# Optimization experiments

Hardware: AMD Instinct MI355X
Metric: run time of the kernel (lower is better)

The kernel has to match this reference:

```python
import jax, jax.numpy as jnp
import numpy as np

B, S, F, H = 4, 1024, 512, 16
D = F // H  # head_dim = 32

def setup_inputs() -> dict:
    key = jax.random.key(0)
    ks = jax.random.split(key, 9)
    init = lambda k, shp: 0.1 * jax.random.normal(k, shp, dtype=jnp.float32)
    return {
        "kv": jax.random.normal(ks[0], (B, S, F), dtype=jnp.float32),
        "q": jax.random.normal(ks[1], (B, S, F), dtype=jnp.float32),
        "mask": jnp.ones((B, 1, S, S), dtype=jnp.int32),
        "Wq": init(ks[2], (F, F)),
        "Wk": init(ks[3], (F, F)),
        "Wv": init(ks[4], (F, F)),
        "Wo": init(ks[5], (F, F)),
        "rel_table": init(ks[6], (2 * S + 1, D)),  # nn.Embed(2*length_q+1, head_dim)
        "Wrel": init(ks[7], (D, D)),  # rel_pos_dense, no bias
    }

def reference(kv, q, mask, Wq, Wk, Wv, Wo, rel_table, Wrel):
    b, s, f = q.shape
    h, d = H, f // H
    qh = (q @ Wq).reshape(b, s, h, d)
    kh = (kv @ Wk).reshape(b, s, h, d)
    vh = (kv @ Wv).reshape(b, s, h, d)
    # raw content scores [b,h,q,k]
    scores = jnp.einsum('bqhd,bkhd->bhqk', qh, kh)
    # relative-position embedding: dist in [0, 2s], table lookup + dense
    dist = jnp.arange(s)[None, :] - jnp.arange(s)[:, None] + s  # [q,k]
    emb = rel_table[dist] @ Wrel  # [q,k,d]
    scores = scores + jnp.einsum('bqhd,qkd->bhqk', qh, emb)
    scores = scores / jnp.sqrt(jnp.asarray(d, scores.dtype))
    # mask-select before softmax (mask [b,1,q,k] broadcast over heads)
    scores = jnp.where(mask > 0, scores, -jnp.inf)
    attn = jax.nn.softmax(scores, axis=-1)
    out = jnp.einsum('bhqk,bkhd->bqhd', attn, vh).reshape(b, s, f)
    return out @ Wo  # dropout is identity (training=False)
```

## Files before the change

kernel.cpp:

```cpp
#include <hip/hip_runtime.h>

#define S_ 1024
#define H_ 16
#define D_ 32

typedef float f32x4 __attribute__((ext_vector_type(4)));
typedef short bf16x8 __attribute__((ext_vector_type(8)));
typedef unsigned long long u64;

static __device__ __forceinline__ short f2b(float f) {
    union { float f; unsigned u; } x; x.f = f;
    unsigned u = x.u;
    unsigned r = u + 0x7fffu + ((u >> 16) & 1u);
    return (short)(r >> 16);
}
static __device__ __forceinline__ unsigned pk_rne(float lo, float hi) {
    union { float f; unsigned u; } a, b; a.f = lo; b.f = hi;
    unsigned ul = a.u + 0x7fffu + ((a.u >> 16) & 1u);
    unsigned uh = b.u + 0x7fffu + ((b.u >> 16) & 1u);
    return __builtin_amdgcn_perm(uh, ul, 0x07060302u);
}
static __device__ __forceinline__ unsigned pk_trunc(float lo, float hi) {
    union { float f; unsigned u; } a, b; a.f = lo; b.f = hi;
    return __builtin_amdgcn_perm(b.u, a.u, 0x07060302u);
}
static __device__ __forceinline__ float bperm(int bidx, float v) {
    union { float f; int i; } x; x.f = v;
    x.i = __builtin_amdgcn_ds_bpermute(bidx, x.i);
    return x.f;
}
static __device__ __forceinline__ int stg64(int row, int c8) {
    return row * 72 + (c8 ^ ((row & 3) << 3));
}

__global__ __launch_bounds__(256)
void prep_kernel(const float* __restrict__ rt, short* __restrict__ relb,
                 const int* __restrict__ mask, u64* __restrict__ mbits,
                 const float* __restrict__ Wq, const float* __restrict__ Wk,
                 const float* __restrict__ Wv, const float* __restrict__ Wo,
                 short* __restrict__ Wt)
{
    __shared__ float ls[32][33];
    int bid = blockIdx.x, t = threadIdx.x;
    if (bid < 257) {
        int i = bid * 256 + t;
        if (i < 2049 * 32) relb[i] = f2b(rt[i]);
        return;
    }
    bid -= 257;
    if (bid < 4096) {
        #pragma unroll
        for (int j = 0; j < 4; ++j) {
            int i = bid * 1024 + j * 256 + t;
            u64 bal = __ballot(mask[i] > 0);
            if ((t & 63) == 0) mbits[i >> 6] = bal;
        }
        return;
    }
    bid -= 4096;
    int mat = bid >> 8, tl = bid & 255, ti = tl >> 4, tj = tl & 15;
    const float* W = (mat == 0) ? Wq : (mat == 1) ? Wk : (mat == 2) ? Wv : Wo;
    int r = t >> 3, c = (t & 7) * 4;
    float4 v = *(const float4*)(W + (long)(ti * 32 + r) * 512 + tj * 32 + c);
    ls[r][c] = v.x; ls[r][c + 1] = v.y; ls[r][c + 2] = v.z; ls[r][c + 3] = v.w;
    __syncthreads();
    int nl = t >> 3, kk = (t & 7) * 4;
    uint2 o = { pk_rne(ls[kk][nl], ls[kk + 1][nl]),
                pk_rne(ls[kk + 2][nl], ls[kk + 3][nl]) };
    *(uint2*)(Wt + ((long)mat * 512 + tj * 32 + nl) * 512 + ti * 32 + kk) = o;
}

__global__ __launch_bounds__(256)
void gemm3_kernel(const float* __restrict__ q, const float* __restrict__ kv,
                  const short* __restrict__ Wt,
                  short* __restrict__ qh, short* __restrict__ kh, short* __restrict__ vt,
                  float scale)
{
    __shared__ __align__(16) short a_s[128 * 72];
    __shared__ __align__(16) short b_s[64 * 72];
    const int t = threadIdx.x;
    const int w = t >> 6, lane = t & 63, l15 = lane & 15, quad = lane >> 4;
    const int wm = w & 1, wn = w >> 1;

    int bid = blockIdx.x;
    const int mat = bid >> 8;
    const int rr_ = bid & 255;
    const int bmr = (rr_ & 31) * 128, bnr = (rr_ >> 5) * 64;
    const float* A = (mat == 0) ? q : kv;
    const short* Wm = Wt + (long)mat * 262144;

    const int srow = t >> 2, scg = (t & 3) << 4;
    f32x4 acc[8] = {};

    for (int k0 = 0; k0 < 512; k0 += 64) {
        #pragma unroll
        for (int hp = 0; hp < 2; ++hp) {
            int row = hp * 64 + srow;
            const float* ap = A + (long)(bmr + row) * 512 + k0 + scg;
            float4 v0 = *(const float4*)(ap);
            float4 v1 = *(const float4*)(ap + 4);
            float4 v2 = *(const float4*)(ap + 8);
            float4 v3 = *(const float4*)(ap + 12);
            uint4 o0 = { pk_rne(v0.x, v0.y), pk_rne(v0.z, v0.w),
                         pk_rne(v1.x, v1.y), pk_rne(v1.z, v1.w) };
            uint4 o1 = { pk_rne(v2.x, v2.y), pk_rne(v2.z, v2.w),
                         pk_rne(v3.x, v3.y), pk_rne(v3.z, v3.w) };
            *(uint4*)(a_s + stg64(row, scg)) = o0;
            *(uint4*)(a_s + stg64(row, scg + 8)) = o1;
        }
        {
            const short* bp = Wm + (long)(bnr + srow) * 512 + k0 + scg;
            *(bf16x8*)(b_s + stg64(srow, scg))     = *(const bf16x8*)(bp);
            *(bf16x8*)(b_s + stg64(srow, scg + 8)) = *(const bf16x8*)(bp + 8);
        }
        __syncthreads();
        bf16x8 af[4][2], bfr[2][2];
        #pragma unroll
        for (int ks = 0; ks < 2; ++ks) {
            #pragma unroll
            for (int i = 0; i < 4; ++i)
                af[i][ks] = *(const bf16x8*)(a_s + stg64(wm * 64 + i * 16 + l15, ks * 32 + quad * 8));
            #pragma unroll
            for (int j = 0; j < 2; ++j)
                bfr[j][ks] = *(const bf16x8*)(b_s + stg64(wn * 32 + j * 16 + l15, ks * 32 + quad * 8));
        }
        if (mat == 2) {
            #pragma unroll
            for (int i = 0; i < 2; ++i)
                #pragma unroll
                for (int j = 0; j < 4; ++j)
                    #pragma unroll
                    for (int ks = 0; ks < 2; ++ks)
                        acc[i * 4 + j] = __builtin_amdgcn_mfma_f32_16x16x32_bf16(bfr[i][ks], af[j][ks], acc[i * 4 + j], 0, 0, 0);
        } else {
            #pragma unroll
            for (int i = 0; i < 4; ++i)
                #pragma unroll
                for (int j = 0; j < 2; ++j)
                    #pragma unroll
                    for (int ks = 0; ks < 2; ++ks)
                        acc[i * 2 + j] = __builtin_amdgcn_mfma_f32_16x16x32_bf16(af[i][ks], bfr[j][ks], acc[i * 2 + j], 0, 0, 0);
        }
        __syncthreads();
    }

    if (mat < 2) {
        short* out = (mat == 0) ? qh : kh;
        float alpha = (mat == 0) ? scale : 1.0f;
        #pragma unroll
        for (int i = 0; i < 4; ++i)
            #pragma unroll
            for (int j = 0; j < 2; ++j)
                #pragma unroll
                for (int r = 0; r < 4; ++r) {
                    int m = bmr + wm * 64 + i * 16 + quad * 4 + r;
                    int n = bnr + wn * 32 + j * 16 + l15;
                    int bb = m >> 10, s = m & 1023, hh = n >> 5, dd = n & 31;
                    out[((long)((bb * 16 + hh) * 1024 + s)) * 32 + dd] = f2b(acc[i * 2 + j][r] * alpha);
                }
    } else {
        #pragma unroll
        for (int i = 0; i < 2; ++i)
            #pragma unroll
            for (int j = 0; j < 4; ++j)
                #pragma unroll
                for (int r = 0; r < 4; ++r) {
                    int n = bnr + wn * 32 + i * 16 + quad * 4 + r;
                    int m = bmr + wm * 64 + j * 16 + l15;
                    int bb = m >> 10, s = m & 1023, hh = n >> 5, dd = n & 31;
                    int sp = (s & ~63) | ((s & 15) << 2) | ((s >> 4) & 3);
                    vt[((long)((bb * 16 + hh) * 32 + dd)) * 1024 + sp] = f2b(acc[i * 4 + j][r]);
                }
    }
}

__global__ __launch_bounds__(256)
void gemm_out_kernel(const short* __restrict__ ao, const short* __restrict__ Wt,
                     float* __restrict__ out)
{
    __shared__ __align__(16) short a_s[64 * 72];
    __shared__ __align__(16) short b_s[64 * 72];
    const int t = threadIdx.x;
    const int w = t >> 6, lane = t & 63, l15 = lane & 15, quad = lane >> 4;
    const int wm = w & 1, wn = w >> 1;
    const int bm = (blockIdx.x & 63) * 64, bn = (blockIdx.x >> 6) * 64;
    const short* Wm = Wt + (long)3 * 262144;
    const int srow = t >> 2, scg = (t & 3) << 4;
    f32x4 acc[2][2] = {};

    for (int k0 = 0; k0 < 512; k0 += 64) {
        {
            const short* apb = ao + (long)(bm + srow) * 512 + k0 + scg;
            *(bf16x8*)(a_s + stg64(srow, scg))     = *(const bf16x8*)(apb);
            *(bf16x8*)(a_s + stg64(srow, scg + 8)) = *(const bf16x8*)(apb + 8);
            const short* bpb = Wm + (long)(bn + srow) * 512 + k0 + scg;
            *(bf16x8*)(b_s + stg64(srow, scg))     = *(const bf16x8*)(bpb);
            *(bf16x8*)(b_s + stg64(srow, scg + 8)) = *(const bf16x8*)(bpb + 8);
        }
        __syncthreads();
        bf16x8 af[2][2], bfr[2][2];
        #pragma unroll
        for (int i = 0; i < 2; ++i)
            #pragma unroll
            for (int ks = 0; ks < 2; ++ks) {
                af[i][ks]  = *(const bf16x8*)(a_s + stg64(wm * 32 + i * 16 + l15, ks * 32 + quad * 8));
                bfr[i][ks] = *(const bf16x8*)(b_s + stg64(wn * 32 + i * 16 + l15, ks * 32 + quad * 8));
            }
        #pragma unroll
        for (int i = 0; i < 2; ++i)
            #pragma unroll
            for (int j = 0; j < 2; ++j)
                #pragma unroll
                for (int ks = 0; ks < 2; ++ks)
                    acc[i][j] = __builtin_amdgcn_mfma_f32_16x16x32_bf16(af[i][ks], bfr[j][ks], acc[i][j], 0, 0, 0);
        __syncthreads();
    }
    #pragma unroll
    for (int i = 0; i < 2; ++i)
        #pragma unroll
        for (int j = 0; j < 2; ++j)
            #pragma unroll
            for (int r = 0; r < 4; ++r) {
                int m = bm + wm * 32 + i * 16 + quad * 4 + r;
                int n = bn + wn * 32 + j * 16 + l15;
                out[(long)m * 512 + n] = acc[i][j][r];
            }
}

__global__ __launch_bounds__(256)
void attn_kernel(const short* __restrict__ qh, const float* __restrict__ wrel,
                 const short* __restrict__ kh, const short* __restrict__ vt,
                 const short* __restrict__ relb, const u64* __restrict__ mbits,
                 short* __restrict__ ao)
{
    __shared__ __align__(16) short smem[4 * 2 * 16 * 72];
    const int t = threadIdx.x;
    const int w = t >> 6, lane = t & 63, l15 = lane & 15, quad = lane >> 4;
    short* pw0 = smem + w * (2 * 16 * 72);
    short* pw1 = pw0 + 16 * 72;

    const int half = w & 1, qsel = w >> 1;
    const int bid = blockIdx.x;
    const int xcd = bid & 7, loc = bid >> 3;
    const int bh = xcd + 8 * (loc >> 5);
    const int qt = (loc & 31) * 2 + qsel;
    const int b = bh >> 4, h = bh & 15;
    const int q0 = qt * 16;
    const int c0 = half * 8;

    const long qbase = ((long)bh * S_ + q0 + l15) * D_ + quad * 8;
    const bf16x8 a_qh = *(const bf16x8*)(qh + qbase);
    const long kv_bh = (long)bh * S_ * D_;
    const u64* mrow = mbits + ((long)b * S_ + q0 + quad * 4) * 16;

    bf16x8 a_qr;
    {
        #pragma unroll
        for (int nt = 0; nt < 2; ++nt) {
            const float* wp = wrel + (long)(nt * 16 + l15) * 32 + quad * 8;
            float4 w0 = *(const float4*)(wp);
            float4 w1 = *(const float4*)(wp + 4);
            bf16x8 bw;
            *(uint4*)&bw = (uint4){ pk_rne(w0.x, w0.y), pk_rne(w0.z, w0.w),
                                    pk_rne(w1.x, w1.y), pk_rne(w1.z, w1.w) };
            f32x4 z = {0.f, 0.f, 0.f, 0.f};
            f32x4 cq = __builtin_amdgcn_mfma_f32_16x16x32_bf16(a_qh, bw, z, 0, 0, 0);
            #pragma unroll
            for (int r = 0; r < 4; ++r)
                pw0[(quad * 4 + r) * 36 + nt * 16 + l15] = f2b(cq[r]);
        }
        asm volatile("" ::: "memory");
        a_qr = *(const bf16x8*)(pw0 + l15 * 36 + quad * 8);
        asm volatile("" ::: "memory");
    }

    int bidx[4];
    #pragma unroll
    for (int r = 0; r < 4; ++r)
        bidx[r] = (quad * 16 + ((l15 + 15 - (quad * 4 + r)) & 15)) * 4;

    f32x4 oacc[2] = {};
    float l4[4] = {0.f, 0.f, 0.f, 0.f};

    bf16x8 preg0 = {}, preg1 = {};
    bf16x8 bv00 = {}, bv01 = {}, bv10 = {}, bv11 = {};

    bf16x8 kf[4], rf[5];
    {
        const int ub0 = c0 * 64 - q0 + (S_ - 15);
        #pragma unroll
        for (int ut = 0; ut < 5; ++ut)
            rf[ut] = *(const bf16x8*)(relb + (long)(ub0 + ut * 16 + l15) * D_ + quad * 8);
        #pragma unroll
        for (int kt = 0; kt < 4; ++kt)
            kf[kt] = *(const bf16x8*)(kh + kv_bh + (long)(c0 * 64 + kt * 16 + l15) * D_ + quad * 8);
    }

    for (int i = 0; i < 8; ++i) {
        const int c = c0 + i;
        const int kbase = c * 64;
        short* pwbuf = (i & 1) ? pw1 : pw0;

        u64 mcur[4];
        #pragma unroll
        for (int r = 0; r < 4; ++r) mcur[r] = mrow[r * 16 + c];

        f32x4 ctf[5], sc[4];
        #pragma unroll
        for (int ut = 0; ut < 5; ++ut) {
            f32x4 z = {0.f, 0.f, 0.f, 0.f};
            ctf[ut] = __builtin_amdgcn_mfma_f32_16x16x32_bf16(a_qr, rf[ut], z, 0, 0, 0);
        }
        #pragma unroll
        for (int kt = 0; kt < 4; ++kt) {
            f32x4 z = {0.f, 0.f, 0.f, 0.f};
            sc[kt] = __builtin_amdgcn_mfma_f32_16x16x32_bf16(a_qh, kf[kt], z, 0, 0, 0);
        }
        if (i) {
            oacc[0] = __builtin_amdgcn_mfma_f32_16x16x32_bf16(preg0, bv00, oacc[0], 0, 0, 0);
            oacc[1] = __builtin_amdgcn_mfma_f32_16x16x32_bf16(preg0, bv01, oacc[1], 0, 0, 0);
            oacc[0] = __builtin_amdgcn_mfma_f32_16x16x32_bf16(preg1, bv10, oacc[0], 0, 0, 0);
            oacc[1] = __builtin_amdgcn_mfma_f32_16x16x32_bf16(preg1, bv11, oacc[1], 0, 0, 0);
        }
        {
            const int cn = c + ((i < 7) ? 1 : 0);
            const int kbn = cn * 64, ubn = kbn - q0 + (S_ - 15);
            #pragma unroll
            for (int ut = 0; ut < 5; ++ut)
                rf[ut] = *(const bf16x8*)(relb + (long)(ubn + ut * 16 + l15) * D_ + quad * 8);
            #pragma unroll
            for (int kt = 0; kt < 4; ++kt)
                kf[kt] = *(const bf16x8*)(kh + kv_bh + (long)(kbn + kt * 16 + l15) * D_ + quad * 8);
        }
        bv00 = *(const bf16x8*)(vt + kv_bh + (long)(l15) * S_ + kbase + quad * 8);
        bv01 = *(const bf16x8*)(vt + kv_bh + (long)(16 + l15) * S_ + kbase + quad * 8);
        bv10 = *(const bf16x8*)(vt + kv_bh + (long)(l15) * S_ + kbase + 32 + quad * 8);
        bv11 = *(const bf16x8*)(vt + kv_bh + (long)(16 + l15) * S_ + kbase + 32 + quad * 8);

        #pragma unroll
        for (int r = 0; r < 4; ++r) {
            int cnd = l15 > quad * 4 + r;
            float tt[5];
            #pragma unroll
            for (int ut = 0; ut < 5; ++ut) tt[ut] = bperm(bidx[r], ctf[ut][r]);
            float s0 = sc[0][r] + (cnd ? tt[1] : tt[0]);
            float s1 = sc[1][r] + (cnd ? tt[2] : tt[1]);
            float s2 = sc[2][r] + (cnd ? tt[3] : tt[2]);
            float s3 = sc[3][r] + (cnd ? tt[4] : tt[3]);
            u64 mw = mcur[r] >> l15;
            unsigned lo = (unsigned)mw, hi = (unsigned)(mw >> 32);
            float p0 = exp2f(s0); p0 = (lo & 1u)         ? p0 : 0.f;
            float p1 = exp2f(s1); p1 = ((lo >> 16) & 1u) ? p1 : 0.f;
            float p2 = exp2f(s2); p2 = (hi & 1u)         ? p2 : 0.f;
            float p3 = exp2f(s3); p3 = ((hi >> 16) & 1u) ? p3 : 0.f;
            l4[r] += (p0 + p1) + (p2 + p3);
            u64 pv = ((u64)pk_trunc(p2, p3) << 32) | (u64)pk_trunc(p0, p1);
            *(u64*)(pwbuf + (quad * 4 + r) * 72 + l15 * 4) = pv;
        }
        asm volatile("" ::: "memory");
        preg0 = *(const bf16x8*)(pwbuf + l15 * 72 + quad * 8);
        preg1 = *(const bf16x8*)(pwbuf + l15 * 72 + 32 + quad * 8);
    }
    oacc[0] = __builtin_amdgcn_mfma_f32_16x16x32_bf16(preg0, bv00, oacc[0], 0, 0, 0);
    oacc[1] = __builtin_amdgcn_mfma_f32_16x16x32_bf16(preg0, bv01, oacc[1], 0, 0, 0);
    oacc[0] = __builtin_amdgcn_mfma_f32_16x16x32_bf16(preg1, bv10, oacc[0], 0, 0, 0);
    oacc[1] = __builtin_amdgcn_mfma_f32_16x16x32_bf16(preg1, bv11, oacc[1], 0, 0, 0);

    #pragma unroll
    for (int r = 0; r < 4; ++r) {
        float l = l4[r];
        l += __shfl_xor(l, 1, 64);
        l += __shfl_xor(l, 2, 64);
        l += __shfl_xor(l, 4, 64);
        l += __shfl_xor(l, 8, 64);
        l4[r] = l;
    }

    asm volatile("" ::: "memory");
    float* fo = (float*)pw0;
    float* fl = (float*)pw1;
    #pragma unroll
    for (int r = 0; r < 4; ++r) {
        #pragma unroll
        for (int dt = 0; dt < 2; ++dt)
            fo[(quad * 4 + r) * 32 + dt * 16 + l15] = oacc[dt][r];
        if (l15 == 0) fl[quad * 4 + r] = l4[r];
    }
    __syncthreads();
    if (half == 0) {
        const float* po = (const float*)(smem + (w ^ 1) * (2 * 16 * 72));
        const float* pl = po + 576;
        #pragma unroll
        for (int r = 0; r < 4; ++r) {
            int row = quad * 4 + r;
            float inv = 1.0f / (l4[r] + pl[row]);
            #pragma unroll
            for (int dt = 0; dt < 2; ++dt) {
                float o = oacc[dt][r] + po[row * 32 + dt * 16 + l15];
                ao[((long)(b * S_ + q0 + row) * H_ + h) * D_ + dt * 16 + l15] = f2b(o * inv);
            }
        }
    }
}

extern "C" void kernel_launch(void* const* d_in, const int* in_sizes, int n_in,
                              void* d_out, int out_size, void* d_ws, size_t ws_size,
                              hipStream_t stream) {
    (void)in_sizes; (void)n_in; (void)out_size; (void)ws_size;
    const float* kv   = (const float*)d_in[0];
    const float* q    = (const float*)d_in[1];
    const int*   mask = (const int*)d_in[2];
    const float* Wq   = (const float*)d_in[3];
    const float* Wk   = (const float*)d_in[4];
    const float* Wv   = (const float*)d_in[5];
    const float* Wo   = (const float*)d_in[6];
    const float* rt   = (const float*)d_in[7];
    const float* Wrel = (const float*)d_in[8];

    char* ws = (char*)d_ws;
    short* qh   = (short*)(ws);
    short* kh   = (short*)(ws + (4u  << 20));
    short* vt   = (short*)(ws + (8u  << 20));
    short* ao   = (short*)(ws + (12u << 20));
    short* Wt   = (short*)(ws + (16u << 20));
    short* relb = (short*)(ws + (18u << 20));
    u64*  mbits = (u64*) (ws + (18u << 20) + (256u << 10));

    const float scale = 0.25503486f;

    prep_kernel<<<257 + 4096 + 1024, 256, 0, stream>>>(
        rt, relb, mask, mbits, Wq, Wk, Wv, Wo, Wt);

    gemm3_kernel<<<768, 256, 0, stream>>>(q, kv, Wt, qh, kh, vt, scale);

    attn_kernel<<<2048, 256, 0, stream>>>(qh, Wrel, kh, vt, relb, mbits, ao);

    gemm_out_kernel<<<512, 256, 0, stream>>>(ao, Wt, (float*)d_out);
}
```

Baseline: 193.3 us.

## Fuse K and V projections per block, enlarge output GEMM tile, simplify attention mapping

The QKV projection kernel now computes K and V together in one block, so the kv activation tile is loaded and converted to bf16 once instead of twice. This cuts the grid from 768 to 512 blocks, with 256 q-blocks and 256 heavier kv-blocks, which leaves the load unbalanced. The output GEMM switches to 128x64 tiles, halving its blocks to raise reuse of the shared-memory tile at the cost of fewer blocks in flight. The attention kernel drops the XCD-aware block remapping for a linear one and reads mask words inline rather than preloading them into registers.

```diff
diff --git a/kernel.cpp b/kernel.cpp
--- a/kernel.cpp
+++ b/kernel.cpp
@@ -77,20 +77,21 @@
                   float scale)
 {
     __shared__ __align__(16) short a_s[128 * 72];
-    __shared__ __align__(16) short b_s[64 * 72];
+    __shared__ __align__(16) short bk_s[64 * 72];
+    __shared__ __align__(16) short bv_s[64 * 72];
     const int t = threadIdx.x;
     const int w = t >> 6, lane = t & 63, l15 = lane & 15, quad = lane >> 4;
     const int wm = w & 1, wn = w >> 1;
 
-    int bid = blockIdx.x;
-    const int mat = bid >> 8;
-    const int rr_ = bid & 255;
-    const int bmr = (rr_ & 31) * 128, bnr = (rr_ >> 5) * 64;
-    const float* A = (mat == 0) ? q : kv;
-    const short* Wm = Wt + (long)mat * 262144;
+    const int bid = blockIdx.x;
+    const int isq = (bid < 256);
+    const int x = isq ? bid : bid - 256;
+    const int bmr = (x & 31) * 128, bnr = (x >> 5) * 64;
+    const float* A = isq ? q : kv;
 
     const int srow = t >> 2, scg = (t & 3) << 4;
     f32x4 acc[8] = {};
+    f32x4 acv[8] = {};
 
     for (int k0 = 0; k0 < 512; k0 += 64) {
         #pragma unroll
@@ -108,13 +109,20 @@
             *(uint4*)(a_s + stg64(row, scg)) = o0;
             *(uint4*)(a_s + stg64(row, scg + 8)) = o1;
         }
-        {
-            const short* bp = Wm + (long)(bnr + srow) * 512 + k0 + scg;
-            *(bf16x8*)(b_s + stg64(srow, scg))     = *(const bf16x8*)(bp);
-            *(bf16x8*)(b_s + stg64(srow, scg + 8)) = *(const bf16x8*)(bp + 8);
+        if (isq) {
+            const short* bp = Wt + (long)(bnr + srow) * 512 + k0 + scg;
+            *(bf16x8*)(bk_s + stg64(srow, scg))     = *(const bf16x8*)(bp);
+            *(bf16x8*)(bk_s + stg64(srow, scg + 8)) = *(const bf16x8*)(bp + 8);
+        } else {
+            const short* bpk = Wt + 262144 + (long)(bnr + srow) * 512 + k0 + scg;
+            const short* bpv = Wt + 2 * 262144 + (long)(bnr + srow) * 512 + k0 + scg;
+            *(bf16x8*)(bk_s + stg64(srow, scg))     = *(const bf16x8*)(bpk);
+            *(bf16x8*)(bk_s + stg64(srow, scg + 8)) = *(const bf16x8*)(bpk + 8);
+            *(bf16x8*)(bv_s + stg64(srow, scg))     = *(const bf16x8*)(bpv);
+            *(bf16x8*)(bv_s + stg64(srow, scg + 8)) = *(const bf16x8*)(bpv + 8);
         }
         __syncthreads();
-        bf16x8 af[4][2], bfr[2][2];
+        bf16x8 af[4][2], bk[2][2];
         #pragma unroll
         for (int ks = 0; ks < 2; ++ks) {
             #pragma unroll
@@ -122,31 +130,36 @@
                 af[i][ks] = *(const bf16x8*)(a_s + stg64(wm * 64 + i * 16 + l15, ks * 32 + quad * 8));
             #pragma unroll
             for (int j = 0; j < 2; ++j)
-                bfr[j][ks] = *(const bf16x8*)(b_s + stg64(wn * 32 + j * 16 + l15, ks * 32 + quad * 8));
-        }
-        if (mat == 2) {
+                bk[j][ks] = *(const bf16x8*)(bk_s + stg64(wn * 32 + j * 16 + l15, ks * 32 + quad * 8));
+        }
+        #pragma unroll
+        for (int i = 0; i < 4; ++i)
+            #pragma unroll
+            for (int j = 0; j < 2; ++j)
+                #pragma unroll
+                for (int ks = 0; ks < 2; ++ks)
+                    acc[i * 2 + j] = __builtin_amdgcn_mfma_f32_16x16x32_bf16(af[i][ks], bk[j][ks], acc[i * 2 + j], 0, 0, 0);
+        if (!isq) {
+            bf16x8 bv_[2][2];
+            #pragma unroll
+            for (int ks = 0; ks < 2; ++ks)
+                #pragma unroll
+                for (int j = 0; j < 2; ++j)
+                    bv_[j][ks] = *(const bf16x8*)(bv_s + stg64(wn * 32 + j * 16 + l15, ks * 32 + quad * 8));
             #pragma unroll
             for (int i = 0; i < 2; ++i)
                 #pragma unroll
                 for (int j = 0; j < 4; ++j)
                     #pragma unroll
                     for (int ks = 0; ks < 2; ++ks)
-                        acc[i * 4 + j] = __builtin_amdgcn_mfma_f32_16x16x32_bf16(bfr[i][ks], af[j][ks], acc[i * 4 + j], 0, 0, 0);
-        } else {
-            #pragma unroll
-            for (int i = 0; i < 4; ++i)
-                #pragma unroll
-                for (int j = 0; j < 2; ++j)
-                    #pragma unroll
-                    for (int ks = 0; ks < 2; ++ks)
-                        acc[i * 2 + j] = __builtin_amdgcn_mfma_f32_16x16x32_bf16(af[i][ks], bfr[j][ks], acc[i * 2 + j], 0, 0, 0);
+                        acv[i * 4 + j] = __builtin_amdgcn_mfma_f32_16x16x32_bf16(bv_[i][ks], af[j][ks], acv[i * 4 + j], 0, 0, 0);
         }
         __syncthreads();
     }
 
-    if (mat < 2) {
-        short* out = (mat == 0) ? qh : kh;
-        float alpha = (mat == 0) ? scale : 1.0f;
+    {
+        short* out = isq ? qh : kh;
+        float alpha = isq ? scale : 1.0f;
         #pragma unroll
         for (int i = 0; i < 4; ++i)
             #pragma unroll
@@ -158,7 +171,8 @@
                     int bb = m >> 10, s = m & 1023, hh = n >> 5, dd = n & 31;
                     out[((long)((bb * 16 + hh) * 1024 + s)) * 32 + dd] = f2b(acc[i * 2 + j][r] * alpha);
                 }
-    } else {
+    }
+    if (!isq) {
         #pragma unroll
         for (int i = 0; i < 2; ++i)
             #pragma unroll
@@ -169,7 +183,7 @@
                     int m = bmr + wm * 64 + j * 16 + l15;
                     int bb = m >> 10, s = m & 1023, hh = n >> 5, dd = n & 31;
                     int sp = (s & ~63) | ((s & 15) << 2) | ((s >> 4) & 3);
-                    vt[((long)((bb * 16 + hh) * 32 + dd)) * 1024 + sp] = f2b(acc[i * 4 + j][r]);
+                    vt[((long)((bb * 16 + hh) * 32 + dd)) * 1024 + sp] = f2b(acv[i * 4 + j][r]);
                 }
     }
 }
@@ -178,52 +192,58 @@
 void gemm_out_kernel(const short* __restrict__ ao, const short* __restrict__ Wt,
                      float* __restrict__ out)
 {
-    __shared__ __align__(16) short a_s[64 * 72];
+    __shared__ __align__(16) short a_s[128 * 72];
     __shared__ __align__(16) short b_s[64 * 72];
     const int t = threadIdx.x;
     const int w = t >> 6, lane = t & 63, l15 = lane & 15, quad = lane >> 4;
     const int wm = w & 1, wn = w >> 1;
-    const int bm = (blockIdx.x & 63) * 64, bn = (blockIdx.x >> 6) * 64;
+    const int bm = (blockIdx.x & 31) * 128, bn = (blockIdx.x >> 5) * 64;
     const short* Wm = Wt + (long)3 * 262144;
     const int srow = t >> 2, scg = (t & 3) << 4;
-    f32x4 acc[2][2] = {};
+    f32x4 acc[8] = {};
 
     for (int k0 = 0; k0 < 512; k0 += 64) {
+        #pragma unroll
+        for (int hp = 0; hp < 2; ++hp) {
+            int row = hp * 64 + srow;
+            const short* apb = ao + (long)(bm + row) * 512 + k0 + scg;
+            *(bf16x8*)(a_s + stg64(row, scg))     = *(const bf16x8*)(apb);
+            *(bf16x8*)(a_s + stg64(row, scg + 8)) = *(const bf16x8*)(apb + 8);
+        }
         {
-            const short* apb = ao + (long)(bm + srow) * 512 + k0 + scg;
-            *(bf16x8*)(a_s + stg64(srow, scg))     = *(const bf16x8*)(apb);
-            *(bf16x8*)(a_s + stg64(srow, scg + 8)) = *(const bf16x8*)(apb + 8);
             const short* bpb = Wm + (long)(bn + srow) * 512 + k0 + scg;
             *(bf16x8*)(b_s + stg64(srow, scg))     = *(const bf16x8*)(bpb);
             *(bf16x8*)(b_s + stg64(srow, scg + 8)) = *(const bf16x8*)(bpb + 8);
         }
         __syncthreads();
-        bf16x8 af[2][2], bfr[2][2];
-        #pragma unroll
-        for (int i = 0; i < 2; ++i)
-            #pragma unroll
-            for (int ks = 0; ks < 2; ++ks) {
-                af[i][ks]  = *(const bf16x8*)(a_s + stg64(wm * 32 + i * 16 + l15, ks * 32 + quad * 8));
-                bfr[i][ks] = *(const bf16x8*)(b_s + stg64(wn * 32 + i * 16 + l15, ks * 32 + quad * 8));
-            }
-        #pragma unroll
-        for (int i = 0; i < 2; ++i)
+        bf16x8 af[4][2], bfr[2][2];
+        #pragma unroll
+        for (int ks = 0; ks < 2; ++ks) {
+            #pragma unroll
+            for (int i = 0; i < 4; ++i)
+                af[i][ks] = *(const bf16x8*)(a_s + stg64(wm * 64 + i * 16 + l15, ks * 32 + quad * 8));
             #pragma unroll
             for (int j = 0; j < 2; ++j)
+                bfr[j][ks] = *(const bf16x8*)(b_s + stg64(wn * 32 + j * 16 + l15, ks * 32 + quad * 8));
+        }
+        #pragma unroll
+        for (int i = 0; i < 4; ++i)
+            #pragma unroll
+            for (int j = 0; j < 2; ++j)
                 #pragma unroll
                 for (int ks = 0; ks < 2; ++ks)
-                    acc[i][j] = __builtin_amdgcn_mfma_f32_16x16x32_bf16(af[i][ks], bfr[j][ks], acc[i][j], 0, 0, 0);
+                    acc[i * 2 + j] = __builtin_amdgcn_mfma_f32_16x16x32_bf16(af[i][ks], bfr[j][ks], acc[i * 2 + j], 0, 0, 0);
         __syncthreads();
     }
     #pragma unroll
-    for (int i = 0; i < 2; ++i)
+    for (int i = 0; i < 4; ++i)
         #pragma unroll
         for (int j = 0; j < 2; ++j)
             #pragma unroll
             for (int r = 0; r < 4; ++r) {
-                int m = bm + wm * 32 + i * 16 + quad * 4 + r;
+                int m = bm + wm * 64 + i * 16 + quad * 4 + r;
                 int n = bn + wn * 32 + j * 16 + l15;
-                out[(long)m * 512 + n] = acc[i][j][r];
+                out[(long)m * 512 + n] = acc[i * 2 + j][r];
             }
 }
 
@@ -240,12 +260,9 @@
     short* pw1 = pw0 + 16 * 72;
 
     const int half = w & 1, qsel = w >> 1;
-    const int bid = blockIdx.x;
-    const int xcd = bid & 7, loc = bid >> 3;
-    const int bh = xcd + 8 * (loc >> 5);
-    const int qt = (loc & 31) * 2 + qsel;
-    const int b = bh >> 4, h = bh & 15;
-    const int q0 = qt * 16;
+    const int gw = blockIdx.x * 2 + qsel;
+    const int qt = gw & 63, h = (gw >> 6) & 15, b = gw >> 10;
+    const int q0 = qt * 16, bh = b * H_ + h;
     const int c0 = half * 8;
 
     const long qbase = ((long)bh * S_ + q0 + l15) * D_ + quad * 8;
@@ -301,10 +318,6 @@
         const int kbase = c * 64;
         short* pwbuf = (i & 1) ? pw1 : pw0;
 
-        u64 mcur[4];
-        #pragma unroll
-        for (int r = 0; r < 4; ++r) mcur[r] = mrow[r * 16 + c];
-
         f32x4 ctf[5], sc[4];
         #pragma unroll
         for (int ut = 0; ut < 5; ++ut) {
@@ -347,7 +360,7 @@
             float s1 = sc[1][r] + (cnd ? tt[2] : tt[1]);
             float s2 = sc[2][r] + (cnd ? tt[3] : tt[2]);
             float s3 = sc[3][r] + (cnd ? tt[4] : tt[3]);
-            u64 mw = mcur[r] >> l15;
+            u64 mw = mrow[r * 16 + c] >> l15;
             unsigned lo = (unsigned)mw, hi = (unsigned)(mw >> 32);
             float p0 = exp2f(s0); p0 = (lo & 1u)         ? p0 : 0.f;
             float p1 = exp2f(s1); p1 = ((lo >> 16) & 1u) ? p1 : 0.f;
@@ -431,9 +444,9 @@
     prep_kernel<<<257 + 4096 + 1024, 256, 0, stream>>>(
         rt, relb, mask, mbits, Wq, Wk, Wv, Wo, Wt);
 
-    gemm3_kernel<<<768, 256, 0, stream>>>(q, kv, Wt, qh, kh, vt, scale);
+    gemm3_kernel<<<512, 256, 0, stream>>>(q, kv, Wt, qh, kh, vt, scale);
 
     attn_kernel<<<2048, 256, 0, stream>>>(qh, Wrel, kh, vt, relb, mbits, ao);
 
-    gemm_out_kernel<<<512, 256, 0, stream>>>(ao, Wt, (float*)d_out);
-}
+    gemm_out_kernel<<<256, 256, 0, stream>>>(ao, Wt, (float*)d_out);
+}
```

New measurement: 198.3 us. +2.6%, slower.

## Move rel-table and mask prep into QKV GEMM launch, simplify attention indexing

Applied to the files above, without the earlier changes.

Splits the prep kernel so only the weight transpose/convert runs first. The rel-table bf16 conversion and mask bit-packing now run as extra blocks of the QKV projection kernel, so that work overlaps the GEMM instead of sitting on the critical path. The attention kernel drops its XCD-aware block remap for a linear mapping, and loads mask words inline instead of prefetching them. It also switches exp2f to __expf and changes the scale from log2e/sqrt(d) to 1/sqrt(d), which keeps the softmax consistent but loses the XCD cache locality.

```diff
diff --git a/kernel.cpp b/kernel.cpp
--- a/kernel.cpp
+++ b/kernel.cpp
@@ -34,30 +34,12 @@
 }
 
 __global__ __launch_bounds__(256)
-void prep_kernel(const float* __restrict__ rt, short* __restrict__ relb,
-                 const int* __restrict__ mask, u64* __restrict__ mbits,
-                 const float* __restrict__ Wq, const float* __restrict__ Wk,
-                 const float* __restrict__ Wv, const float* __restrict__ Wo,
-                 short* __restrict__ Wt)
+void prepw_kernel(const float* __restrict__ Wq, const float* __restrict__ Wk,
+                  const float* __restrict__ Wv, const float* __restrict__ Wo,
+                  short* __restrict__ Wt)
 {
     __shared__ float ls[32][33];
     int bid = blockIdx.x, t = threadIdx.x;
-    if (bid < 257) {
-        int i = bid * 256 + t;
-        if (i < 2049 * 32) relb[i] = f2b(rt[i]);
-        return;
-    }
-    bid -= 257;
-    if (bid < 4096) {
-        #pragma unroll
-        for (int j = 0; j < 4; ++j) {
-            int i = bid * 1024 + j * 256 + t;
-            u64 bal = __ballot(mask[i] > 0);
-            if ((t & 63) == 0) mbits[i >> 6] = bal;
-        }
-        return;
-    }
-    bid -= 4096;
     int mat = bid >> 8, tl = bid & 255, ti = tl >> 4, tj = tl & 15;
     const float* W = (mat == 0) ? Wq : (mat == 1) ? Wk : (mat == 2) ? Wv : Wo;
     int r = t >> 3, c = (t & 7) * 4;
@@ -74,15 +56,34 @@
 void gemm3_kernel(const float* __restrict__ q, const float* __restrict__ kv,
                   const short* __restrict__ Wt,
                   short* __restrict__ qh, short* __restrict__ kh, short* __restrict__ vt,
-                  float scale)
+                  float scale,
+                  const float* __restrict__ rt, short* __restrict__ relb,
+                  const int* __restrict__ mask, u64* __restrict__ mbits)
 {
     __shared__ __align__(16) short a_s[128 * 72];
     __shared__ __align__(16) short b_s[64 * 72];
     const int t = threadIdx.x;
+    int bid = blockIdx.x;
+
+    if (bid >= 768) {
+        bid -= 768;
+        if (bid < 257) {
+            int i = bid * 256 + t;
+            if (i < 2049 * 32) relb[i] = f2b(rt[i]);
+            return;
+        }
+        bid -= 257;
+        #pragma unroll
+        for (int j = 0; j < 4; ++j) {
+            int i = bid * 1024 + j * 256 + t;
+            u64 bal = __ballot(mask[i] > 0);
+            if ((t & 63) == 0) mbits[i >> 6] = bal;
+        }
+        return;
+    }
+
     const int w = t >> 6, lane = t & 63, l15 = lane & 15, quad = lane >> 4;
     const int wm = w & 1, wn = w >> 1;
-
-    int bid = blockIdx.x;
     const int mat = bid >> 8;
     const int rr_ = bid & 255;
     const int bmr = (rr_ & 31) * 128, bnr = (rr_ >> 5) * 64;
@@ -240,12 +241,9 @@
     short* pw1 = pw0 + 16 * 72;
 
     const int half = w & 1, qsel = w >> 1;
-    const int bid = blockIdx.x;
-    const int xcd = bid & 7, loc = bid >> 3;
-    const int bh = xcd + 8 * (loc >> 5);
-    const int qt = (loc & 31) * 2 + qsel;
-    const int b = bh >> 4, h = bh & 15;
-    const int q0 = qt * 16;
+    const int gw = blockIdx.x * 2 + qsel;
+    const int qt = gw & 63, h = (gw >> 6) & 15, b = gw >> 10;
+    const int q0 = qt * 16, bh = b * H_ + h;
     const int c0 = half * 8;
 
     const long qbase = ((long)bh * S_ + q0 + l15) * D_ + quad * 8;
@@ -301,10 +299,6 @@
         const int kbase = c * 64;
         short* pwbuf = (i & 1) ? pw1 : pw0;
 
-        u64 mcur[4];
-        #pragma unroll
-        for (int r = 0; r < 4; ++r) mcur[r] = mrow[r * 16 + c];
-
         f32x4 ctf[5], sc[4];
         #pragma unroll
         for (int ut = 0; ut < 5; ++ut) {
@@ -347,12 +341,12 @@
             float s1 = sc[1][r] + (cnd ? tt[2] : tt[1]);
             float s2 = sc[2][r] + (cnd ? tt[3] : tt[2]);
             float s3 = sc[3][r] + (cnd ? tt[4] : tt[3]);
-            u64 mw = mcur[r] >> l15;
+            u64 mw = mrow[r * 16 + c] >> l15;
             unsigned lo = (unsigned)mw, hi = (unsigned)(mw >> 32);
-            float p0 = exp2f(s0); p0 = (lo & 1u)         ? p0 : 0.f;
-            float p1 = exp2f(s1); p1 = ((lo >> 16) & 1u) ? p1 : 0.f;
-            float p2 = exp2f(s2); p2 = (hi & 1u)         ? p2 : 0.f;
-            float p3 = exp2f(s3); p3 = ((hi >> 16) & 1u) ? p3 : 0.f;
+            float p0 = __expf(s0); p0 = (lo & 1u)         ? p0 : 0.f;
+            float p1 = __expf(s1); p1 = ((lo >> 16) & 1u) ? p1 : 0.f;
+            float p2 = __expf(s2); p2 = (hi & 1u)         ? p2 : 0.f;
+            float p3 = __expf(s3); p3 = ((hi >> 16) & 1u) ? p3 : 0.f;
             l4[r] += (p0 + p1) + (p2 + p3);
             u64 pv = ((u64)pk_trunc(p2, p3) << 32) | (u64)pk_trunc(p0, p1);
             *(u64*)(pwbuf + (quad * 4 + r) * 72 + l15 * 4) = pv;
@@ -426,12 +420,12 @@
     short* relb = (short*)(ws + (18u << 20));
     u64*  mbits = (u64*) (ws + (18u << 20) + (256u << 10));
 
-    const float scale = 0.25503486f;
-
-    prep_kernel<<<257 + 4096 + 1024, 256, 0, stream>>>(
-        rt, relb, mask, mbits, Wq, Wk, Wv, Wo, Wt);
-
-    gemm3_kernel<<<768, 256, 0, stream>>>(q, kv, Wt, qh, kh, vt, scale);
+    const float scale = 0.17677669529663687f;
+
+    prepw_kernel<<<1024, 256, 0, stream>>>(Wq, Wk, Wv, Wo, Wt);
+
+    gemm3_kernel<<<768 + 257 + 4096, 256, 0, stream>>>(
+        q, kv, Wt, qh, kh, vt, scale, rt, relb, mask, mbits);
 
     attn_kernel<<<2048, 256, 0, stream>>>(qh, Wrel, kh, vt, relb, mbits, ao);
 
```

New measurement: 198.1 us. 2.5% more time.
